# Optimization experiments

Measured on AMD Instinct MI355X. Metric: run time of the kernel, lower is better.

## Reference

```python
import jax, jax.numpy as jnp
import numpy as np

K, D, R = 12, 8192, 16   # num cores, categorical dim per core, TR rank
B = 65536                # batch of multi-indices


def setup_inputs() -> dict:
    key = jax.random.key(0)
    k_idx, k_cores = jax.random.split(key)
    index = jax.random.randint(k_idx, (B, K), 0, D, dtype=jnp.int32)
    # log-space core parameters; softplus'd on the fly (see TRCategorical.cores)
    log_cores = jax.random.normal(k_cores, (K, D, R, R), dtype=jnp.float32) * 0.5
    return {"index": index, "log_cores": log_cores}


def reference(index, log_cores):
    """trip_index_log_prob: log p(index) under the tensor-ring categorical."""
    cores = jax.nn.softplus(log_cores)              # [K, D, R, R], positive
    # running per-sample head product and normalizer chain
    prob = cores[0][index[:, 0]]                    # [B, R, R] gather
    norm = cores[0].sum(axis=0)                     # [R, R]
    for k in range(1, K):                           # fixed small K, sequential by construction
        prob = prob @ cores[k][index[:, k]]         # [B,R,R] @ [B,R,R]
        norm = norm @ cores[k].sum(axis=0)
    log_num = jnp.log(jnp.trace(prob, axis1=1, axis2=2))   # [B]
    log_Z = jnp.log(jnp.trace(norm))                        # scalar
    return log_num - log_Z
```

## Files before the change

kernel.cpp:

```cpp
#include <hip/hip_runtime.h>
#include <cstdint>
#include <cstddef>

typedef float f4 __attribute__((ext_vector_type(4)));

#define KCORES 12
#define DCAT   8192
#define RR     256

#define WS_LOGZ  0
#define WS_NORM  256
#define WS_TABLE 16384
#define TABLE_BYTES ((size_t)KCORES * DCAT * RR * 4ull)
#define NEED_SP (WS_TABLE + TABLE_BYTES)

__device__ __forceinline__ float softplus_f(float x) {
    return fmaxf(x, 0.0f) + log1pf(expf(-fabsf(x)));
}

__device__ __forceinline__ void softplus4(f4& v) {
    v[0] = softplus_f(v[0]); v[1] = softplus_f(v[1]);
    v[2] = softplus_f(v[2]); v[3] = softplus_f(v[3]);
}

template<bool WRITE_TABLE>
__global__ __launch_bounds__(256)
void sp_norm_kernel(const float* __restrict__ lc, float* __restrict__ table,
                    float* __restrict__ norm) {
    int blk = blockIdx.x;
    int k = blk >> 7;
    int p = blk & 127;
    int t = threadIdx.x;
    int w = t >> 6, lane = t & 63;
    size_t base = ((size_t)k * DCAT + (size_t)p * 64) * RR;
    const f4* in4 = (const f4*)(lc + base);
    f4* out4 = WRITE_TABLE ? (f4*)(table + base) : nullptr;
    f4 acc = {0.f, 0.f, 0.f, 0.f};
    #pragma unroll
    for (int it = 0; it < 16; ++it) {
        f4 v = in4[it * 256 + t];
        softplus4(v);
        if (WRITE_TABLE) out4[it * 256 + t] = v;
        acc += v;
    }
    __shared__ f4 red[4][64];
    red[w][lane] = acc;
    __syncthreads();
    if (w == 0) {
        f4 s = red[0][lane] + red[1][lane] + red[2][lane] + red[3][lane];
        float* nk = norm + k * RR + lane * 4;
        atomicAdd(nk + 0, s[0]);
        atomicAdd(nk + 1, s[1]);
        atomicAdd(nk + 2, s[2]);
        atomicAdd(nk + 3, s[3]);
    }
}

__global__ __launch_bounds__(256)
void chain_kernel(const float* __restrict__ norm, float* __restrict__ logZ) {
    __shared__ float A[16][17];
    __shared__ float Bm[16][17];
    __shared__ float red[256];
    int t = threadIdx.x;
    int i = t >> 4, j = t & 15;
    float logscale = 0.f;
    A[i][j] = norm[i * 16 + j];
    __syncthreads();
    for (int k = 1; k < KCORES; ++k) {
        Bm[i][j] = norm[k * RR + i * 16 + j];
        __syncthreads();
        float s = 0.f;
        #pragma unroll
        for (int r = 0; r < 16; ++r) s += A[i][r] * Bm[r][j];
        red[t] = s;
        __syncthreads();
        #pragma unroll
        for (int off = 128; off >= 1; off >>= 1) {
            if (t < off) red[t] = fmaxf(red[t], red[t + off]);
            __syncthreads();
        }
        float mx = red[0];
        A[i][j] = s / mx;
        if (t == 0) logscale += logf(mx);
        __syncthreads();
    }
    if (t == 0) {
        float tr = 0.f;
        #pragma unroll
        for (int r = 0; r < 16; ++r) tr += A[r][r];
        *logZ = logf(tr) + logscale;
    }
}

template<int Q>
__device__ __forceinline__ f4 quad_bcast(f4 v) {
    f4 r;
    #pragma unroll
    for (int c = 0; c < 4; ++c) {
        int x = __builtin_bit_cast(int, v[c]);
        x = __builtin_amdgcn_mov_dpp(x, Q * 0x55, 0xF, 0xF, false);
        r[c] = __builtin_bit_cast(float, x);
    }
    return r;
}

#define QSTEP(Q) { f4 crow = quad_bcast<Q>(cur);            \
    acc += crow[0] * mb[(4*(Q)+0)*4 + j4];                  \
    acc += crow[1] * mb[(4*(Q)+1)*4 + j4];                  \
    acc += crow[2] * mb[(4*(Q)+2)*4 + j4];                  \
    acc += crow[3] * mb[(4*(Q)+3)*4 + j4]; }

template<bool SP>
__global__ __launch_bounds__(256)
void trip_kernel(const int* __restrict__ index, const float* __restrict__ table,
                 const float* __restrict__ logZ, float* __restrict__ out, int B) {
    __shared__ f4 mbuf[2][4][64];
    int w = threadIdx.x >> 6;
    int lane = threadIdx.x & 63;
    int b = blockIdx.x * 4 + w;
    bool live = (b < B);
    int j4 = lane & 3;

    int myidx = 0;
    if (live && lane < KCORES) myidx = index[b * KCORES + lane];

    const f4* t4 = (const f4*)table;

    int d0 = __builtin_amdgcn_readlane(myidx, 0);
    f4 cur = t4[(size_t)d0 * 64 + lane];
    if (!SP) softplus4(cur);

    int d1 = __builtin_amdgcn_readlane(myidx, 1);
    f4 nxt = t4[((size_t)DCAT + d1) * 64 + lane];
    if (!SP) softplus4(nxt);

    #pragma unroll
    for (int k = 1; k < KCORES; ++k) {
        int p = (k - 1) & 1;
        mbuf[p][w][lane] = nxt;
        if (k + 1 < KCORES) {
            int dn = __builtin_amdgcn_readlane(myidx, k + 1);
            nxt = t4[((size_t)(k + 1) * DCAT + dn) * 64 + lane];
            if (!SP) softplus4(nxt);
        }
        asm volatile("s_waitcnt lgkmcnt(0)" ::: "memory");
        const f4* mb = &mbuf[p][w][0];
        f4 acc = {0.f, 0.f, 0.f, 0.f};
        QSTEP(0) QSTEP(1) QSTEP(2) QSTEP(3)
        cur = acc;
    }

    int i = lane >> 2;
    float contrib = 0.f;
    if ((i >> 2) == j4) contrib = cur[i & 3];
    #pragma unroll
    for (int off = 32; off >= 1; off >>= 1) contrib += __shfl_xor(contrib, off);
    if (live && lane == 0) out[b] = logf(contrib) - *logZ;
}

extern "C" void kernel_launch(void* const* d_in, const int* in_sizes, int n_in,
                              void* d_out, int out_size, void* d_ws, size_t ws_size,
                              hipStream_t stream) {
    const int*   index = (const int*)d_in[0];
    const float* lc    = (const float*)d_in[1];
    float* out = (float*)d_out;
    char*  ws  = (char*)d_ws;
    float* logZ  = (float*)(ws + WS_LOGZ);
    float* norm  = (float*)(ws + WS_NORM);
    float* table = (float*)(ws + WS_TABLE);

    int B = in_sizes[0] / KCORES;
    int nblk = (B + 3) / 4;

    hipMemsetAsync(norm, 0, KCORES * RR * sizeof(float), stream);

    bool sp = (ws_size >= NEED_SP);
    if (sp) {
        sp_norm_kernel<true><<<KCORES * 128, 256, 0, stream>>>(lc, table, norm);
        chain_kernel<<<1, 256, 0, stream>>>(norm, logZ);
        trip_kernel<true><<<nblk, 256, 0, stream>>>(index, table, logZ, out, B);
    } else {
        sp_norm_kernel<false><<<KCORES * 128, 256, 0, stream>>>(lc, nullptr, norm);
        chain_kernel<<<1, 256, 0, stream>>>(norm, logZ);
        trip_kernel<false><<<nblk, 256, 0, stream>>>(index, lc, logZ, out, B);
    }
}
```

Measured before the change: 328.2 us.

## Store softplus table as transposed bf16 and chain products with MFMA

The preprocessing kernel now writes the softplus'd core table as bf16 in a transposed layout, which halves the bytes written and the bytes gathered per sample. The per-sample product chain switches from a DPP/LDS FP32 matrix-vector scheme to bf16 MFMA 16x16x32 instructions. Between steps the running product is passed through shuffles in bf16, and all 12 core gathers are issued up front. This risks precision loss from rounding the intermediates to bf16 across 12 chained multiplies, wastes half of each MFMA's K dimension, and drops the fallback path for a small workspace.

```diff
diff --git a/kernel.cpp b/kernel.cpp
--- a/kernel.cpp
+++ b/kernel.cpp
@@ -3,6 +3,9 @@
 #include <cstddef>
 
 typedef float f4 __attribute__((ext_vector_type(4)));
+typedef short bf16x8 __attribute__((ext_vector_type(8)));
+typedef unsigned int u32;
+typedef u32 u32x4 __attribute__((ext_vector_type(4)));
 
 #define KCORES 12
 #define DCAT   8192
@@ -11,48 +14,57 @@
 #define WS_LOGZ  0
 #define WS_NORM  256
 #define WS_TABLE 16384
-#define TABLE_BYTES ((size_t)KCORES * DCAT * RR * 4ull)
-#define NEED_SP (WS_TABLE + TABLE_BYTES)
 
 __device__ __forceinline__ float softplus_f(float x) {
     return fmaxf(x, 0.0f) + log1pf(expf(-fabsf(x)));
 }
 
-__device__ __forceinline__ void softplus4(f4& v) {
-    v[0] = softplus_f(v[0]); v[1] = softplus_f(v[1]);
-    v[2] = softplus_f(v[2]); v[3] = softplus_f(v[3]);
+__device__ __forceinline__ u32 cvt_pk_bf16(float lo, float hi) {
+    u32 r;
+    asm("v_cvt_pk_bf16_f32 %0, %1, %2" : "=v"(r) : "v"(lo), "v"(hi));
+    return r;
 }
 
-template<bool WRITE_TABLE>
 __global__ __launch_bounds__(256)
-void sp_norm_kernel(const float* __restrict__ lc, float* __restrict__ table,
-                    float* __restrict__ norm) {
+void sp_norm_mt(const float* __restrict__ lc, unsigned short* __restrict__ table,
+                float* __restrict__ norm) {
+    __shared__ float sm[16 * 256];
+    __shared__ f4 red[4][64];
     int blk = blockIdx.x;
-    int k = blk >> 7;
-    int p = blk & 127;
     int t = threadIdx.x;
     int w = t >> 6, lane = t & 63;
-    size_t base = ((size_t)k * DCAT + (size_t)p * 64) * RR;
-    const f4* in4 = (const f4*)(lc + base);
-    f4* out4 = WRITE_TABLE ? (f4*)(table + base) : nullptr;
+    int k = blk >> 9;
+    const f4* in4 = (const f4*)lc + (size_t)blk * 1024;
+    f4* sm4 = (f4*)sm;
     f4 acc = {0.f, 0.f, 0.f, 0.f};
     #pragma unroll
-    for (int it = 0; it < 16; ++it) {
+    for (int it = 0; it < 4; ++it) {
         f4 v = in4[it * 256 + t];
-        softplus4(v);
-        if (WRITE_TABLE) out4[it * 256 + t] = v;
+        v[0] = softplus_f(v[0]); v[1] = softplus_f(v[1]);
+        v[2] = softplus_f(v[2]); v[3] = softplus_f(v[3]);
+        sm4[it * 256 + t] = v;
         acc += v;
     }
-    __shared__ f4 red[4][64];
     red[w][lane] = acc;
     __syncthreads();
     if (w == 0) {
         f4 s = red[0][lane] + red[1][lane] + red[2][lane] + red[3][lane];
         float* nk = norm + k * RR + lane * 4;
-        atomicAdd(nk + 0, s[0]);
-        atomicAdd(nk + 1, s[1]);
-        atomicAdd(nk + 2, s[2]);
-        atomicAdd(nk + 3, s[3]);
+        atomicAdd(nk + 0, s[0]); atomicAdd(nk + 1, s[1]);
+        atomicAdd(nk + 2, s[2]); atomicAdd(nk + 3, s[3]);
+    }
+    #pragma unroll
+    for (int it2 = 0; it2 < 2; ++it2) {
+        int e  = it2 * 2048 + t * 8;
+        int mo = e >> 8, p = e & 255;
+        int i  = p >> 4, j0 = p & 15;
+        const float* base = sm + mo * 256 + j0 * 16 + i;
+        float v0 = base[0],   v1 = base[16],  v2 = base[32],  v3 = base[48];
+        float v4 = base[64],  v5 = base[80],  v6 = base[96],  v7 = base[112];
+        u32x4 wv;
+        wv.x = cvt_pk_bf16(v0, v1); wv.y = cvt_pk_bf16(v2, v3);
+        wv.z = cvt_pk_bf16(v4, v5); wv.w = cvt_pk_bf16(v6, v7);
+        *(u32x4*)(table + (size_t)blk * 4096 + e) = wv;
     }
 }
 
@@ -92,67 +104,59 @@
     }
 }
 
-template<int Q>
-__device__ __forceinline__ f4 quad_bcast(f4 v) {
-    f4 r;
-    #pragma unroll
-    for (int c = 0; c < 4; ++c) {
-        int x = __builtin_bit_cast(int, v[c]);
-        x = __builtin_amdgcn_mov_dpp(x, Q * 0x55, 0xF, 0xF, false);
-        r[c] = __builtin_bit_cast(float, x);
-    }
-    return r;
-}
-
-#define QSTEP(Q) { f4 crow = quad_bcast<Q>(cur);            \
-    acc += crow[0] * mb[(4*(Q)+0)*4 + j4];                  \
-    acc += crow[1] * mb[(4*(Q)+1)*4 + j4];                  \
-    acc += crow[2] * mb[(4*(Q)+2)*4 + j4];                  \
-    acc += crow[3] * mb[(4*(Q)+3)*4 + j4]; }
-
-template<bool SP>
 __global__ __launch_bounds__(256)
-void trip_kernel(const int* __restrict__ index, const float* __restrict__ table,
-                 const float* __restrict__ logZ, float* __restrict__ out, int B) {
-    __shared__ f4 mbuf[2][4][64];
-    int w = threadIdx.x >> 6;
-    int lane = threadIdx.x & 63;
+void trip_mfma(const int* __restrict__ index, const unsigned short* __restrict__ table,
+               const float* __restrict__ logZ, float* __restrict__ out, int B) {
+    int w = threadIdx.x >> 6, lane = threadIdx.x & 63;
     int b = blockIdx.x * 4 + w;
     bool live = (b < B);
-    int j4 = lane & 3;
+    int g = lane >> 4, c = lane & 15;
 
     int myidx = 0;
-    if (live && lane < KCORES) myidx = index[b * KCORES + lane];
+    if (live && lane < KCORES) myidx = index[(size_t)b * KCORES + lane];
 
-    const f4* t4 = (const f4*)table;
-
-    int d0 = __builtin_amdgcn_readlane(myidx, 0);
-    f4 cur = t4[(size_t)d0 * 64 + lane];
-    if (!SP) softplus4(cur);
-
-    int d1 = __builtin_amdgcn_readlane(myidx, 1);
-    f4 nxt = t4[((size_t)DCAT + d1) * 64 + lane];
-    if (!SP) softplus4(nxt);
-
+    u32x4 afr[KCORES];
     #pragma unroll
-    for (int k = 1; k < KCORES; ++k) {
-        int p = (k - 1) & 1;
-        mbuf[p][w][lane] = nxt;
-        if (k + 1 < KCORES) {
-            int dn = __builtin_amdgcn_readlane(myidx, k + 1);
-            nxt = t4[((size_t)(k + 1) * DCAT + dn) * 64 + lane];
-            if (!SP) softplus4(nxt);
+    for (int k = 0; k < KCORES; ++k) {
+        int d = __builtin_amdgcn_readlane(myidx, k);
+        u32x4 a = {0u, 0u, 0u, 0u};
+        if (lane < 32) {
+            const u32x4* src = (const u32x4*)(table + (((size_t)k * DCAT + d) << 8));
+            a = src[(c << 1) | g];
         }
-        asm volatile("s_waitcnt lgkmcnt(0)" ::: "memory");
-        const f4* mb = &mbuf[p][w][0];
-        f4 acc = {0.f, 0.f, 0.f, 0.f};
-        QSTEP(0) QSTEP(1) QSTEP(2) QSTEP(3)
-        cur = acc;
+        afr[k] = a;
     }
 
-    int i = lane >> 2;
+    u32 bw0 = 0, bw1 = 0, bw2 = 0, bw3 = 0;
+    if ((c >> 3) == g) {
+        int j = c - 8 * g;
+        u32 val = 0x3F80u << (16 * (j & 1));
+        if ((j >> 1) == 0) bw0 = val; else if ((j >> 1) == 1) bw1 = val;
+        else if ((j >> 1) == 2) bw2 = val; else bw3 = val;
+    }
+
+    f4 acc = {0.f, 0.f, 0.f, 0.f};
+    #pragma unroll
+    for (int k = 0; k < KCORES; ++k) {
+        u32x4 bv = {bw0, bw1, bw2, bw3};
+        bf16x8 af = __builtin_bit_cast(bf16x8, afr[k]);
+        bf16x8 bf = __builtin_bit_cast(bf16x8, bv);
+        f4 z = {0.f, 0.f, 0.f, 0.f};
+        acc = __builtin_amdgcn_mfma_f32_16x16x32_bf16(af, bf, z, 0, 0, 0);
+        if (k < KCORES - 1) {
+            u32 p0 = cvt_pk_bf16(acc[0], acc[1]);
+            u32 p1 = cvt_pk_bf16(acc[2], acc[3]);
+            int s0 = (g << 5) | c;
+            int s1 = s0 + 16;
+            bw0 = (u32)__shfl((int)p0, s0);
+            bw1 = (u32)__shfl((int)p1, s0);
+            bw2 = (u32)__shfl((int)p0, s1);
+            bw3 = (u32)__shfl((int)p1, s1);
+        }
+    }
+
     float contrib = 0.f;
-    if ((i >> 2) == j4) contrib = cur[i & 3];
+    if ((c >> 2) == g) contrib = acc[c & 3];
     #pragma unroll
     for (int off = 32; off >= 1; off >>= 1) contrib += __shfl_xor(contrib, off);
     if (live && lane == 0) out[b] = logf(contrib) - *logZ;
@@ -161,27 +165,19 @@
 extern "C" void kernel_launch(void* const* d_in, const int* in_sizes, int n_in,
                               void* d_out, int out_size, void* d_ws, size_t ws_size,
                               hipStream_t stream) {
-    const int*   index = (const int*)d_in[0];
-    const float* lc    = (const float*)d_in[1];
+    const int*   idx = (const int*)d_in[0];
+    const float* lc  = (const float*)d_in[1];
     float* out = (float*)d_out;
     char*  ws  = (char*)d_ws;
-    float* logZ  = (float*)(ws + WS_LOGZ);
-    float* norm  = (float*)(ws + WS_NORM);
-    float* table = (float*)(ws + WS_TABLE);
+    float* logZ = (float*)(ws + WS_LOGZ);
+    float* norm = (float*)(ws + WS_NORM);
+    unsigned short* table = (unsigned short*)(ws + WS_TABLE);
 
     int B = in_sizes[0] / KCORES;
     int nblk = (B + 3) / 4;
 
     hipMemsetAsync(norm, 0, KCORES * RR * sizeof(float), stream);
-
-    bool sp = (ws_size >= NEED_SP);
-    if (sp) {
-        sp_norm_kernel<true><<<KCORES * 128, 256, 0, stream>>>(lc, table, norm);
-        chain_kernel<<<1, 256, 0, stream>>>(norm, logZ);
-        trip_kernel<true><<<nblk, 256, 0, stream>>>(index, table, logZ, out, B);
-    } else {
-        sp_norm_kernel<false><<<KCORES * 128, 256, 0, stream>>>(lc, nullptr, norm);
-        chain_kernel<<<1, 256, 0, stream>>>(norm, logZ);
-        trip_kernel<false><<<nblk, 256, 0, stream>>>(index, lc, logZ, out, B);
-    }
+    sp_norm_mt<<<KCORES * DCAT / 16, 256, 0, stream>>>(lc, table, norm);
+    chain_kernel<<<1, 256, 0, stream>>>(norm, logZ);
+    trip_mfma<<<nblk, 256, 0, stream>>>(idx, table, logZ, out, B);
 }
```

Measured after the change: 330.7 us. About the same (+0.8%).
